# Kernel optimization log

Hardware: AMD Instinct MI355X
Metric: run time of the kernel (lower is better)

Reference implementation:

```python
import jax, jax.numpy as jnp
import numpy as np

B, N, STRIDE, NSAMPLE, RADIUS = 2, 8192, 4, 32, 0.1
CIN, COUT, LPC = 64, 128, 16
M = N // STRIDE
EPS = 1e-5


def conv1d(x, W, b=None):
    y = jnp.einsum('oc,bcn->bon', W, x)
    return y + b[None, :, None] if b is not None else y


def conv2d(x, W, b=None):
    y = jnp.einsum('oc,bcmk->bomk', W, x)
    return y + b[None, :, None, None] if b is not None else y


def bn(x, prm):
    # prm: [4, C] = (gamma, beta, running_mean, running_var); inference BN
    sh = (1, -1) + (1,) * (x.ndim - 2)
    g, be, m, v = (prm[i].reshape(sh) for i in range(4))
    return (x - m) * jax.lax.rsqrt(v + EPS) * g + be


def fps(p, m):
    # furthest point sampling, p: [B,N,3] -> idx [B,m] int32 (starts at index 0)
    b, n, _ = p.shape
    first = jnp.zeros((b,), jnp.int32)
    d0 = jnp.full((b, n), 1e10, p.dtype)

    def step(carry, _):
        dist, last = carry
        lastp = jnp.take_along_axis(p, jnp.broadcast_to(last[:, None, None], (b, 1, 3)), axis=1)
        dist = jnp.minimum(dist, jnp.sum((p - lastp) ** 2, -1))
        nxt = jnp.argmax(dist, -1).astype(jnp.int32)
        return (dist, nxt), nxt

    _, rest = jax.lax.scan(step, (d0, first), None, length=m - 1)
    return jnp.concatenate([first[:, None], rest.T], axis=1)


def ball_query(q, s, radius, ns):
    # q [B,M,3], s [B,N,3] -> neighbor indices [B,M,ns] (first ns points within radius, padded with first hit)
    n = s.shape[1]
    sqd = jnp.sum((q[:, :, None, :] - s[:, None, :, :]) ** 2, -1)  # [B,M,N]
    cand = jnp.where(sqd < radius * radius, jnp.arange(n, dtype=jnp.int32)[None, None, :], n)
    srt = jnp.sort(cand, axis=-1)[:, :, :ns]
    first = srt[:, :, :1]
    return jnp.where(srt == n, first, srt)


def group(feat, gidx):
    # feat [B,C,N], gidx [B,M,ns] -> [B,C,M,ns]
    return jax.vmap(lambda ft, gi: ft[:, gi])(feat, gidx)


def setup_inputs() -> dict:
    key = jax.random.key(0)
    ks = jax.random.split(key, 24)

    def w(k_, o, i):
        return jax.random.normal(k_, (o, i), jnp.float32) / np.sqrt(i).astype(np.float32)

    def bnp(k_, c):  # positive gamma/var, small-ish beta/mean
        return jax.random.uniform(k_, (4, c), jnp.float32) + 0.1

    return {
        'p': jax.random.uniform(ks[0], (B, N, 3), jnp.float32),
        'lp': jax.random.normal(ks[1], (B, LPC, N), jnp.float32),
        'f': jax.random.normal(ks[2], (B, CIN, N), jnp.float32),
        'W_skip': w(ks[3], COUT, CIN), 'b_skip': jax.random.normal(ks[4], (COUT,), jnp.float32) * 0.02,
        'W_post': w(ks[5], COUT, CIN), 'bn_post': bnp(ks[6], COUT),
        'W_loc1': w(ks[7], 32, LPC), 'bn_loc1': bnp(ks[8], 32),
        'W_loc2': w(ks[9], COUT, 32), 'bn_loc2': bnp(ks[10], COUT),
        'W_g': w(ks[11], 1, CIN), 'b_g': jax.random.normal(ks[12], (1,), jnp.float32) * 0.02,
        'W_v': w(ks[13], CIN, CIN), 'b_v': jax.random.normal(ks[14], (CIN,), jnp.float32) * 0.02,
        'W_w1': w(ks[15], CIN // 4, CIN), 'bn_w1': bnp(ks[16], CIN // 4),
        'W_w2': w(ks[17], CIN, CIN // 4), 'b_w2': jax.random.normal(ks[18], (CIN,), jnp.float32) * 0.02,
        'W_m': w(ks[19], COUT, CIN), 'bn_m': bnp(ks[20], COUT),
    }


def reference(p, lp, f, W_skip, b_skip, W_post, bn_post, W_loc1, bn_loc1, W_loc2, bn_loc2,
              W_g, b_g, W_v, b_v, W_w1, bn_w1, W_w2, b_w2, W_m, bn_m):
    b, n = p.shape[0], p.shape[1]
    m = n // STRIDE
    relu = jax.nn.relu

    # --- sampling + gathers ---
    idx = fps(p, m)  # [B,M]
    new_p = jnp.take_along_axis(p, jnp.broadcast_to(idx[:, :, None], (b, m, 3)), axis=1)
    fi = jnp.take_along_axis(f, jnp.broadcast_to(idx[:, None, :], (b, f.shape[1], m)), axis=2)
    lpi = jnp.take_along_axis(lp, jnp.broadcast_to(idx[:, None, :], (b, lp.shape[1], m)), axis=2)
    identity = conv1d(fi, W_skip, b_skip)  # [B,COUT,M]

    # --- global top-k relative-position attention branch ---
    att = jax.nn.sigmoid(conv1d(fi, W_g, b_g))  # [B,1,M]
    k = min(m // 4, 160)
    _, index_k = jax.lax.top_k(att[:, 0, :], k)  # [B,k]
    sparse_f = jnp.take_along_axis(fi, jnp.broadcast_to(index_k[:, None, :], (b, fi.shape[1], k)), axis=2)
    v = conv1d(sparse_f, W_v, b_v)  # [B,CIN,k]
    fi_att = fi * att
    r_qk = fi_att[:, :, :, None] - sparse_f[:, :, None, :]  # [B,CIN,M,k]
    r_qk = relu(bn(conv2d(r_qk, W_w1), bn_w1))
    r_qk = conv2d(r_qk, W_w2, b_w2)
    w_ = relu(r_qk)
    attfeat = jnp.mean(w_ * v[:, :, None, :], axis=-1)  # [B,CIN,M]
    global_f = relu(bn(conv1d(attfeat - fi, W_m), bn_m))  # [B,COUT,M]

    # --- local grouping branch ---
    fpost = relu(bn(conv1d(f, W_post), bn_post))  # [B,COUT,N]
    lpf = jnp.concatenate([lp, fpost], axis=1)  # [B,LPC+COUT,N]
    gidx = ball_query(new_p, p, RADIUS, NSAMPLE)  # [B,M,ns]
    lpfj = group(lpf, gidx)  # [B,LPC+COUT,M,ns]
    lpj, fj = lpfj[:, :LPC], lpfj[:, LPC:]
    dlpj = lpj - lpi[:, :, :, None]
    loc = relu(bn(conv2d(dlpj, W_loc1), bn_loc1))
    loc = relu(bn(conv2d(loc, W_loc2), bn_loc2))
    fout = jnp.max(fj + loc, axis=-1)  # [B,COUT,M]
    fout = fout + global_f
    fout = relu(fout + identity)
    return new_p, lpi, fout
```

## Files before the change

### kernel.cpp

```cpp
#include <hip/hip_runtime.h>
#include <stdint.h>

#define BB 2
#define NN 8192
#define MM 2048
#define CIN_ 64
#define COUT_ 128
#define LPC_ 16
#define NS_ 32
#define KSEL 160
#define EPSB 1e-5f

#define WS_IDX    0
#define WS_IDXK   4096
#define WS_LOGIT  4416
#define WS_ATT    8512
#define WS_FLAG   16380
#define WS_FIT    16384
#define WS_IDT    278528
#define WS_A1S    802816
#define WS_VT     868352
#define WS_B1S    888832
#define WS_GFT    893952
#define WS_FPOST  1418240
#define WS_GIDX   3515392

#define OUT_NEWP 0
#define OUT_LPI  12288
#define OUT_F    77824

typedef float    f16v __attribute__((ext_vector_type(16)));
typedef unsigned u16v __attribute__((ext_vector_type(16)));
typedef int      i16v __attribute__((ext_vector_type(16)));
typedef unsigned u8v  __attribute__((ext_vector_type(8)));

__device__ __forceinline__ float dist2_rn(float ax, float ay, float az,
                                          float bx, float by, float bz) {
  float dx = __fsub_rn(ax, bx);
  float dy = __fsub_rn(ay, by);
  float dz = __fsub_rn(az, bz);
  return __fadd_rn(__fadd_rn(__fmul_rn(dx, dx), __fmul_rn(dy, dy)), __fmul_rn(dz, dz));
}

template <int CTRL>
__device__ __forceinline__ unsigned long long dppmax64(unsigned long long x) {
  unsigned lo = (unsigned)x, hi = (unsigned)(x >> 32);
  unsigned plo = (unsigned)__builtin_amdgcn_update_dpp(0, (int)lo, CTRL, 0xF, 0xF, true);
  unsigned phi = (unsigned)__builtin_amdgcn_update_dpp(0, (int)hi, CTRL, 0xF, 0xF, true);
  unsigned long long o = ((unsigned long long)phi << 32) | plo;
  return o > x ? o : x;
}
#define DPP_XOR1 0xB1
#define DPP_XOR2 0x4E
#define DPP_HALFMIR 0x141
#define DPP_MIR 0x140
#define DPP_BC15 0x142
#define DPP_BC31 0x143

__device__ __forceinline__ unsigned mort4(unsigned x) {
  return (x & 1u) | ((x & 2u) << 2) | ((x & 4u) << 4) | ((x & 8u) << 6);
}

#define PPT 16
#define FPS_T 512
#define NWAVE 8
#define FPOST_BLKS ((BB * NN * 16) / FPS_T)
#define WARM_BLKS 254
#define WARM_CAP 4000

__global__ __launch_bounds__(FPS_T) void k_fps_fpost(const float* __restrict__ p,
                                                     int* __restrict__ idx_out,
                                                     float* __restrict__ newp_out,
                                                     const float* __restrict__ f,
                                                     const float* __restrict__ Wpost,
                                                     const float* __restrict__ bnpost,
                                                     float* __restrict__ fpostT,
                                                     int* __restrict__ flag) {
  __shared__ union {
    struct { unsigned int hist[4096]; unsigned int perm[NN]; } s;
    struct { float newp[MM * 3]; int idx[MM]; } o;
  } u;
  __shared__ unsigned long long slots[2][NWAVE];
  __shared__ float4 slotc[2][NWAVE];
  __shared__ unsigned int wsum[NWAVE];

  if (blockIdx.x >= 2 + FPOST_BLKS) {
    float a = 1.0000001f;
    float acc = (float)threadIdx.x;
    for (int it = 0; it < WARM_CAP; ++it) {
      if (__hip_atomic_load(flag, __ATOMIC_RELAXED, __HIP_MEMORY_SCOPE_AGENT) >= 2) break;
      #pragma unroll 64
      for (int k = 0; k < 512; ++k) acc = __builtin_fmaf(acc, a, 1.0f);
    }
    asm volatile("" ::"v"(acc));
    return;
  }

  if (blockIdx.x >= 2) {
    int gt = (blockIdx.x - 2) * FPS_T + threadIdx.x;
    int og = gt & 15, nn = gt >> 4;
    int b = nn >> 13, n = nn & 8191;
    const float* fb = f + b * CIN_ * NN + n;
    float acc[8];
    #pragma unroll
    for (int q = 0; q < 8; q++) acc[q] = 0.f;
    for (int c = 0; c < 64; c++) {
      float x = fb[c * NN];
      #pragma unroll
      for (int q = 0; q < 8; q++) acc[q] = fmaf(Wpost[(og * 8 + q) * 64 + c], x, acc[q]);
    }
    #pragma unroll
    for (int q = 0; q < 8; q++) {
      int o = og * 8 + q;
      float ga = bnpost[o], be = bnpost[COUT_ + o], mu = bnpost[2 * COUT_ + o],
            va = bnpost[3 * COUT_ + o];
      float sc = ga / sqrtf(va + EPSB);
      fpostT[(b * NN + n) * 128 + o] = fmaxf(acc[q] * sc + (be - mu * sc), 0.f);
    }
    return;
  }

  const int b = blockIdx.x;
  if (threadIdx.x == 0)
    __hip_atomic_store(flag, 0, __ATOMIC_RELAXED, __HIP_MEMORY_SCOPE_AGENT);
  const float* pb = p + b * NN * 3;
  const int tid = threadIdx.x;
  const int lane = tid & 63;
  const int wid = tid >> 6;

  for (int i = tid; i < 4096; i += FPS_T) u.s.hist[i] = 0u;
  __syncthreads();

  i16v cellv;
  #pragma unroll
  for (int k = 0; k < PPT; k++) {
    int i = tid + k * FPS_T;
    float x = pb[i * 3 + 0], y = pb[i * 3 + 1], z = pb[i * 3 + 2];
    int cx = (int)(x * 16.f); cx = cx < 0 ? 0 : (cx > 15 ? 15 : cx);
    int cy = (int)(y * 16.f); cy = cy < 0 ? 0 : (cy > 15 ? 15 : cy);
    int cz = (int)(z * 16.f); cz = cz < 0 ? 0 : (cz > 15 ? 15 : cz);
    int c = (int)(mort4((unsigned)cx) | (mort4((unsigned)cy) << 1) |
                  (mort4((unsigned)cz) << 2));
    cellv[k] = c;
    atomicAdd(&u.s.hist[c], 1u);
  }
  __syncthreads();

  u8v h;
  unsigned int s = 0;
  #pragma unroll
  for (int k = 0; k < 8; k++) { h[k] = u.s.hist[tid * 8 + k]; s += h[k]; }
  unsigned int pre = s;
  for (int d = 1; d < 64; d <<= 1) {
    unsigned int o = (unsigned int)__shfl_up((int)pre, d);
    if (lane >= d) pre += o;
  }
  if (lane == 63) wsum[wid] = pre;
  __syncthreads();
  if (tid < NWAVE) {
    unsigned int v = wsum[tid];
    unsigned int q = v;
    for (int d = 1; d < NWAVE; d <<= 1) {
      unsigned int o = (unsigned int)__shfl_up((int)q, d);
      if (tid >= d) q += o;
    }
    wsum[tid] = q - v;
  }
  __syncthreads();
  unsigned int base = wsum[wid] + (pre - s);
  #pragma unroll
  for (int k = 0; k < 8; k++) {
    u.s.hist[tid * 8 + k] = base;
    base += h[k];
  }
  __syncthreads();

  #pragma unroll
  for (int k = 0; k < PPT; k++) {
    unsigned int pos = atomicAdd(&u.s.hist[cellv[k]], 1u);
    u.s.perm[pos] = (unsigned int)(tid + k * FPS_T);
  }
  __syncthreads();

  f16v sx, sy, sz, dist;
  u16v lov;
  float bxmin = 1e30f, bymin = 1e30f, bzmin = 1e30f;
  float bxmax = -1e30f, bymax = -1e30f, bzmax = -1e30f;
  #pragma unroll
  for (int q = 0; q < PPT; q++) {
    unsigned int o = u.s.perm[tid * PPT + q];
    float x = pb[o * 3 + 0], y = pb[o * 3 + 1], z = pb[o * 3 + 2];
    sx[q] = x; sy[q] = y; sz[q] = z;
    lov[q] = ((8191u - o) << 4) | (unsigned int)q;
    dist[q] = 1e10f;
    bxmin = fminf(bxmin, x); bxmax = fmaxf(bxmax, x);
    bymin = fminf(bymin, y); bymax = fmaxf(bymax, y);
    bzmin = fminf(bzmin, z); bzmax = fmaxf(bzmax, z);
  }

  float wx = pb[0], wy = pb[1], wz = pb[2];
  unsigned long long thrPack = ((unsigned long long)__float_as_uint(1e10f) << 32);
  unsigned long long wpCache = 0ull;
  float scX = 0.f, scY = 0.f, scZ = 0.f;
  bool isPub = false;
  __syncthreads();

  if (tid == 0) {
    u.o.newp[0] = wx; u.o.newp[1] = wy; u.o.newp[2] = wz;
    u.o.idx[0] = 0;
  }

  for (int t = 1; t < MM; t++) {
    const int buf = t & 1;
    float ex = fmaxf(fmaxf(bxmin - wx, wx - bxmax), 0.f);
    float ey = fmaxf(fmaxf(bymin - wy, wy - bymax), 0.f);
    float ez = fmaxf(fmaxf(bzmin - wz, wz - bzmax), 0.f);
    float bd = (ex * ex + ey * ey + ez * ez) * 0.999f;
    float thrMax = __uint_as_float((unsigned int)(thrPack >> 32));
    bool active = (bd < thrMax);
    unsigned long long wmask = __ballot(active);
    if (wmask) {
      if (active) {
        unsigned long long best = 0ull;
        #pragma unroll
        for (int q = 0; q < PPT; q++) {
          float d = dist2_rn(sx[q], sy[q], sz[q], wx, wy, wz);
          float nd = fminf(dist[q], d);
          dist[q] = nd;
          unsigned long long pk =
              ((unsigned long long)__float_as_uint(nd) << 32) | (unsigned long long)lov[q];
          best = pk > best ? pk : best;
        }
        thrPack = best;
      }
      unsigned long long wp = thrPack;
      wp = dppmax64<DPP_XOR1>(wp);
      wp = dppmax64<DPP_XOR2>(wp);
      wp = dppmax64<DPP_HALFMIR>(wp);
      wp = dppmax64<DPP_MIR>(wp);
      wp = dppmax64<DPP_BC15>(wp);
      wp = dppmax64<DPP_BC31>(wp);
      unsigned wlo = (unsigned)__builtin_amdgcn_readlane((int)(unsigned)wp, 63);
      unsigned whi = (unsigned)__builtin_amdgcn_readlane((int)(unsigned)(wp >> 32), 63);
      unsigned long long wmax = ((unsigned long long)whi << 32) | wlo;
      isPub = (thrPack == wmax);
      if (isPub) {
        wpCache = wmax;
        unsigned qs = (unsigned)(wmax & 15ull);
        #pragma unroll
        for (int q = 0; q < PPT; q++) {
          if (qs == (unsigned)q) { scX = sx[q]; scY = sy[q]; scZ = sz[q]; }
        }
      }
    }
    if (isPub) {
      slots[buf][wid] = wpCache;
      slotc[buf][wid] = make_float4(scX, scY, scZ, 0.f);
    }
    __syncthreads();

    int sidx = lane & (NWAVE - 1);
    unsigned long long sp = slots[buf][sidx];
    float4 sc = slotc[buf][sidx];
    unsigned long long w2 = sp;
    w2 = dppmax64<DPP_XOR1>(w2);
    w2 = dppmax64<DPP_XOR2>(w2);
    w2 = dppmax64<DPP_HALFMIR>(w2);
    unsigned long long bal = __ballot(sp == w2);
    int src = __ffsll(bal) - 1;
    wx = __shfl(sc.x, src);
    wy = __shfl(sc.y, src);
    wz = __shfl(sc.z, src);
    if (tid == 0) {
      int worig = 8191 - (int)((w2 >> 4) & 0x1FFFull);
      u.o.newp[t * 3 + 0] = wx;
      u.o.newp[t * 3 + 1] = wy;
      u.o.newp[t * 3 + 2] = wz;
      u.o.idx[t] = worig;
    }
  }
  __syncthreads();

  for (int i = tid; i < MM * 3; i += FPS_T) newp_out[b * MM * 3 + i] = u.o.newp[i];
  for (int i = tid; i < MM; i += FPS_T) idx_out[b * MM + i] = u.o.idx[i];
  __syncthreads();
  if (tid == 0)
    __hip_atomic_fetch_add(flag, 1, __ATOMIC_RELEASE, __HIP_MEMORY_SCOPE_AGENT);
}

__global__ __launch_bounds__(256) void k_gather(const float* __restrict__ lp,
                                                const float* __restrict__ f,
                                                const int* __restrict__ idx,
                                                const float* __restrict__ Wg,
                                                const float* __restrict__ bg,
                                                float* __restrict__ fiT,
                                                float* __restrict__ logit,
                                                float* __restrict__ att,
                                                float* __restrict__ out_lpi) {
  int gm = blockIdx.x * 256 + threadIdx.x;
  if (gm >= BB * MM) return;
  int b = gm >> 11, m = gm & 2047;
  int j = idx[gm];
  const float* lpb = lp + b * LPC_ * NN;
  float* olpi = out_lpi + b * LPC_ * MM;
  #pragma unroll
  for (int c = 0; c < LPC_; c++) olpi[c * MM + m] = lpb[c * NN + j];
  const float* fb = f + b * CIN_ * NN;
  float lg = bg[0];
  #pragma unroll
  for (int c = 0; c < CIN_; c++) {
    float x = fb[c * NN + j];
    fiT[gm * 64 + c] = x;
    lg = __fadd_rn(lg, __fmul_rn(Wg[c], x));
  }
  logit[gm] = lg;
  att[gm] = 1.f / (1.f + expf(-lg));
}

__global__ __launch_bounds__(256) void k_ident(const float* __restrict__ fiT,
                                               const float* __restrict__ Wskip,
                                               const float* __restrict__ bskip,
                                               float* __restrict__ idT) {
  int gt = blockIdx.x * 256 + threadIdx.x;
  if (gt >= BB * MM * 16) return;
  int og = gt & 15, gm = gt >> 4;
  const float* fvp = fiT + gm * 64;
  #pragma unroll
  for (int q = 0; q < 8; q++) {
    int o = og * 8 + q;
    float a = bskip[o];
    #pragma unroll
    for (int c = 0; c < 64; c++) a = fmaf(Wskip[o * 64 + c], fvp[c], a);
    idT[gm * 128 + o] = a;
  }
}

__global__ __launch_bounds__(1024) void k_topk(const float* __restrict__ att,
                                               int* __restrict__ idxk) {
  __shared__ unsigned long long key[MM];
  int b = blockIdx.x, tid = threadIdx.x;
  for (int i = tid; i < MM; i += 1024) {
    unsigned int u = __float_as_uint(att[b * MM + i]);
    u ^= (u & 0x80000000u) ? 0xFFFFFFFFu : 0x80000000u;
    u = ~u;
    key[i] = ((unsigned long long)u << 32) | (unsigned int)i;
  }
  __syncthreads();
  for (int k = 2; k <= MM; k <<= 1) {
    for (int j = k >> 1; j > 0; j >>= 1) {
      for (int i = tid; i < MM; i += 1024) {
        int ixj = i ^ j;
        if (ixj > i) {
          bool up = (i & k) == 0;
          unsigned long long a = key[i], c = key[ixj];
          if ((a > c) == up) { key[i] = c; key[ixj] = a; }
        }
      }
      __syncthreads();
    }
  }
  if (tid < KSEL) idxk[b * KSEL + tid] = (int)(key[tid] & 0xFFFFFFFFull);
}

__global__ __launch_bounds__(256) void k_a1s(const float* __restrict__ fiT,
                                             const float* __restrict__ att,
                                             const float* __restrict__ Ww1,
                                             const float* __restrict__ bnw1,
                                             float* __restrict__ a1sT) {
  int gm = blockIdx.x * 256 + threadIdx.x;
  if (gm >= BB * MM) return;
  const float* fvp = fiT + gm * 64;
  float a = att[gm];
  #pragma unroll
  for (int c1 = 0; c1 < 16; c1++) {
    float acc = 0.f;
    #pragma unroll
    for (int c = 0; c < 64; c++) acc = fmaf(Ww1[c1 * 64 + c], fvp[c] * a, acc);
    float g = bnw1[c1], be = bnw1[16 + c1], mu = bnw1[32 + c1], va = bnw1[48 + c1];
    float sc = g / sqrtf(va + EPSB);
    a1sT[gm * 16 + c1] = acc * sc + (be - mu * sc);
  }
}

__global__ __launch_bounds__(256) void k_vb1(const float* __restrict__ fiT,
                                             const int* __restrict__ idxk,
                                             const float* __restrict__ Wv,
                                             const float* __restrict__ bv,
                                             const float* __restrict__ Ww1,
                                             const float* __restrict__ bnw1,
                                             float* __restrict__ vT,
                                             float* __restrict__ b1sT) {
  int gk = blockIdx.x * 256 + threadIdx.x;
  if (gk >= BB * KSEL) return;
  int b = gk / KSEL;
  int kk = idxk[gk];
  const float* fvp = fiT + (b * MM + kk) * 64;
  for (int o = 0; o < 64; o++) {
    float acc = bv[o];
    #pragma unroll
    for (int c = 0; c < 64; c++) acc = fmaf(Wv[o * 64 + c], fvp[c], acc);
    vT[gk * 64 + o] = acc;
  }
  #pragma unroll
  for (int c1 = 0; c1 < 16; c1++) {
    float acc = 0.f;
    #pragma unroll
    for (int c = 0; c < 64; c++) acc = fmaf(Ww1[c1 * 64 + c], fvp[c], acc);
    float g = bnw1[c1], va = bnw1[48 + c1];
    b1sT[gk * 16 + c1] = acc * (g / sqrtf(va + EPSB));
  }
}

__global__ __launch_bounds__(256) void k_att(const float* __restrict__ a1sT,
                                             const float* __restrict__ b1sT,
                                             const float* __restrict__ vT,
                                             const float* __restrict__ fiT,
                                             const float* __restrict__ Ww2,
                                             const float* __restrict__ bw2,
                                             const float* __restrict__ Wm,
                                             const float* __restrict__ bnm,
                                             float* __restrict__ gfT) {
  __shared__ float B1sh[KSEL * 16];
  __shared__ float dsh[4][64];
  int b = blockIdx.x >> 9;
  const float* bsrc = b1sT + b * KSEL * 16;
  for (int i = threadIdx.x; i < KSEL * 16; i += 256) B1sh[i] = bsrc[i];
  __syncthreads();
  int wid = threadIdx.x >> 6, lane = threadIdx.x & 63;
  int gm = blockIdx.x * 4 + wid;
  int c15 = lane & 15;
  float a1 = a1sT[gm * 16 + c15];
  f16v wrow;
  #pragma unroll
  for (int c = 0; c < 16; c++) wrow[c] = Ww2[lane * 16 + c];
  float bw = bw2[lane];
  const float* vp = vT + b * KSEL * 64 + lane;
  float acc = 0.f;
  for (int k = 0; k < KSEL; k++) {
    float t = fmaxf(a1 - B1sh[k * 16 + c15], 0.f);
    float r2 = bw;
    #pragma unroll
    for (int c = 0; c < 16; c++) {
      float tc = __int_as_float(__builtin_amdgcn_readlane(__float_as_int(t), c));
      r2 = fmaf(wrow[c], tc, r2);
    }
    acc = fmaf(fmaxf(r2, 0.f), vp[k * 64], acc);
  }
  float af = acc * (1.f / (float)KSEL);
  float d = af - fiT[gm * 64 + lane];
  dsh[wid][lane] = d;
  __syncthreads();
  #pragma unroll
  for (int t2 = 0; t2 < 2; t2++) {
    int o = lane + t2 * 64;
    float g = 0.f;
    #pragma unroll
    for (int c = 0; c < 64; c++) g = fmaf(Wm[o * 64 + c], dsh[wid][c], g);
    float ga = bnm[o], be = bnm[COUT_ + o], mu = bnm[2 * COUT_ + o], va = bnm[3 * COUT_ + o];
    float sc = ga / sqrtf(va + EPSB);
    gfT[gm * 128 + o] = fmaxf(g * sc + (be - mu * sc), 0.f);
  }
}

__global__ __launch_bounds__(256) void k_ball(const float* __restrict__ p,
                                              const float* __restrict__ newp,
                                              int* __restrict__ gidx) {
  int wid = threadIdx.x >> 6, lane = threadIdx.x & 63;
  int gm = blockIdx.x * 4 + wid;
  int b = gm >> 11;
  const float* q = newp + gm * 3;
  float qx = q[0], qy = q[1], qz = q[2];
  const float* pb = p + b * NN * 3;
  int* out = gidx + gm * NS_;
  const float RR = (float)(0.1 * 0.1);
  int cnt = 0, firstj = 0;
  bool haveFirst = false;
  for (int chunk = 0; chunk < NN / 64 && cnt < NS_; chunk++) {
    int j = chunk * 64 + lane;
    float d = dist2_rn(qx, qy, qz, pb[j * 3], pb[j * 3 + 1], pb[j * 3 + 2]);
    unsigned long long mask = __ballot(d < RR);
    while (mask && cnt < NS_) {
      int l = __ffsll(mask) - 1;
      mask &= mask - 1;
      int jj = chunk * 64 + l;
      if (!haveFirst) { firstj = jj; haveFirst = true; }
      if (lane == 0) out[cnt] = jj;
      cnt++;
    }
  }
  if (lane == 0) {
    for (int i = cnt; i < NS_; i++) out[i] = firstj;
  }
}

__global__ __launch_bounds__(128) void k_final(const float* __restrict__ lp,
                                               const float* __restrict__ lpi_out,
                                               const int* __restrict__ gidx,
                                               const float* __restrict__ Wl1,
                                               const float* __restrict__ bnl1,
                                               const float* __restrict__ Wl2,
                                               const float* __restrict__ bnl2,
                                               const float* __restrict__ fpostT,
                                               const float* __restrict__ gfT,
                                               const float* __restrict__ idT,
                                               float* __restrict__ out_f) {
  __shared__ float loc1[NS_][32];
  __shared__ float dls[NS_][16];
  int gm = blockIdx.x;
  int b = gm >> 11, m = gm & 2047;
  int tid = threadIdx.x;
  const int* gx = gidx + gm * NS_;
  for (int i = tid; i < NS_ * 16; i += 128) {
    int s = i >> 4, c = i & 15;
    int j = gx[s];
    dls[s][c] = lp[(b * LPC_ + c) * NN + j] - lpi_out[(b * LPC_ + c) * MM + m];
  }
  __syncthreads();
  for (int i = tid; i < NS_ * 32; i += 128) {
    int s = i >> 5, o = i & 31;
    float a = 0.f;
    #pragma unroll
    for (int c = 0; c < 16; c++) a = fmaf(Wl1[o * 16 + c], dls[s][c], a);
    float ga = bnl1[o], be = bnl1[32 + o], mu = bnl1[64 + o], va = bnl1[96 + o];
    float sc = ga / sqrtf(va + EPSB);
    loc1[s][o] = fmaxf(a * sc + (be - mu * sc), 0.f);
  }
  __syncthreads();
  f16v wr0, wr1;
  #pragma unroll
  for (int c = 0; c < 16; c++) { wr0[c] = Wl2[tid * 32 + c]; wr1[c] = Wl2[tid * 32 + 16 + c]; }
  float ga = bnl2[tid], be = bnl2[128 + tid], mu = bnl2[256 + tid], va = bnl2[384 + tid];
  float sc = ga / sqrtf(va + EPSB);
  float sh = be - mu * sc;
  float mx = -1e30f;
  for (int s = 0; s < NS_; s++) {
    float g = 0.f;
    #pragma unroll
    for (int c = 0; c < 16; c++) g = fmaf(wr0[c], loc1[s][c], g);
    #pragma unroll
    for (int c = 0; c < 16; c++) g = fmaf(wr1[c], loc1[s][16 + c], g);
    float l2 = fmaxf(g * sc + sh, 0.f);
    int j = gx[s];
    float fj = fpostT[(b * NN + j) * 128 + tid];
    mx = fmaxf(mx, fj + l2);
  }
  float fout = fmaxf(mx + gfT[gm * 128 + tid] + idT[gm * 128 + tid], 0.f);
  out_f[(b * COUT_ + tid) * MM + m] = fout;
}

extern "C" void kernel_launch(void* const* d_in, const int* in_sizes, int n_in,
                              void* d_out, int out_size, void* d_ws, size_t ws_size,
                              hipStream_t stream) {
  (void)in_sizes; (void)n_in; (void)out_size; (void)ws_size;
  const float* p      = (const float*)d_in[0];
  const float* lp     = (const float*)d_in[1];
  const float* f      = (const float*)d_in[2];
  const float* W_skip = (const float*)d_in[3];
  const float* b_skip = (const float*)d_in[4];
  const float* W_post = (const float*)d_in[5];
  const float* bn_post= (const float*)d_in[6];
  const float* W_loc1 = (const float*)d_in[7];
  const float* bn_loc1= (const float*)d_in[8];
  const float* W_loc2 = (const float*)d_in[9];
  const float* bn_loc2= (const float*)d_in[10];
  const float* W_g    = (const float*)d_in[11];
  const float* b_g    = (const float*)d_in[12];
  const float* W_v    = (const float*)d_in[13];
  const float* b_v    = (const float*)d_in[14];
  const float* W_w1   = (const float*)d_in[15];
  const float* bn_w1  = (const float*)d_in[16];
  const float* W_w2   = (const float*)d_in[17];
  const float* b_w2   = (const float*)d_in[18];
  const float* W_m    = (const float*)d_in[19];
  const float* bn_m   = (const float*)d_in[20];

  float* out = (float*)d_out;
  float* ws = (float*)d_ws;
  int*   idx    = (int*)(ws + WS_IDX);
  int*   idxk   = (int*)(ws + WS_IDXK);
  float* att    = ws + WS_ATT;
  int*   flag   = (int*)(ws + WS_FLAG);
  float* fiT    = ws + WS_FIT;
  float* idT    = ws + WS_IDT;
  float* a1sT   = ws + WS_A1S;
  float* vT     = ws + WS_VT;
  float* b1sT   = ws + WS_B1S;
  float* gfT    = ws + WS_GFT;
  float* fpostT = ws + WS_FPOST;
  float* logit  = ws + WS_LOGIT;
  int*   gidx   = (int*)(ws + WS_GIDX);

  k_fps_fpost<<<2 + FPOST_BLKS + WARM_BLKS, FPS_T, 0, stream>>>(p, idx, out + OUT_NEWP, f,
                                                                W_post, bn_post, fpostT, flag);
  k_gather<<<(BB * MM + 255) / 256, 256, 0, stream>>>(lp, f, idx, W_g, b_g, fiT, logit, att,
                                                      out + OUT_LPI);
  k_ident<<<(BB * MM * 16) / 256, 256, 0, stream>>>(fiT, W_skip, b_skip, idT);
  k_topk<<<BB, 1024, 0, stream>>>(att, idxk);
  k_a1s<<<(BB * MM + 255) / 256, 256, 0, stream>>>(fiT, att, W_w1, bn_w1, a1sT);
  k_vb1<<<(BB * KSEL + 255) / 256, 256, 0, stream>>>(fiT, idxk, W_v, b_v, W_w1, bn_w1, vT, b1sT);
  k_att<<<(BB * MM) / 4, 256, 0, stream>>>(a1sT, b1sT, vT, fiT, W_w2, b_w2, W_m, bn_m, gfT);
  k_ball<<<(BB * MM) / 4, 256, 0, stream>>>(p, out + OUT_NEWP, gidx);
  k_final<<<BB * MM, 128, 0, stream>>>(lp, out + OUT_LPI, gidx, W_loc1, bn_loc1, W_loc2, bn_loc2,
                                       fpostT, gfT, idT, out + OUT_F);
}
```

Measured before the change: 2.295 ms.

## Keep FPS point coordinates in LDS and look up winner by packed slot

Moves the sorted point coordinates out of per-thread registers into shared memory (xy as float2, z separately). The packed key now carries the owning thread and slot, so after the block-wide max every lane reads the winner's coordinates straight from LDS. This removes the coordinate-publish slots, the ballot/shuffle broadcast and the per-wave select loop. It also splits the per-thread max into four independent chains and moves the new_p output write into the gather kernel. The aim is to shorten each serial FPS iteration and lower register pressure, at the cost of extra LDS reads in the inner loop.

Result: no change. 2.324 ms (+1.3%).

```diff
diff --git a/kernel.cpp b/kernel.cpp
--- a/kernel.cpp
+++ b/kernel.cpp
@@ -70,18 +70,21 @@
 
 __global__ __launch_bounds__(FPS_T) void k_fps_fpost(const float* __restrict__ p,
                                                      int* __restrict__ idx_out,
-                                                     float* __restrict__ newp_out,
                                                      const float* __restrict__ f,
                                                      const float* __restrict__ Wpost,
                                                      const float* __restrict__ bnpost,
                                                      float* __restrict__ fpostT,
                                                      int* __restrict__ flag) {
-  __shared__ union {
-    struct { unsigned int hist[4096]; unsigned int perm[NN]; } s;
-    struct { float newp[MM * 3]; int idx[MM]; } o;
-  } u;
+  __shared__ float2 xyl[NN];
+  __shared__ union UZ {
+    float zz[NN];
+    struct { float zlow[NN - 4096]; unsigned short perm[NN]; } s;
+  } uz;
+  __shared__ union UH {
+    unsigned int hist[4096];
+    int idxs[MM];
+  } uh;
   __shared__ unsigned long long slots[2][NWAVE];
-  __shared__ float4 slotc[2][NWAVE];
   __shared__ unsigned int wsum[NWAVE];
 
   if (blockIdx.x >= 2 + FPOST_BLKS) {
@@ -128,7 +131,7 @@
   const int lane = tid & 63;
   const int wid = tid >> 6;
 
-  for (int i = tid; i < 4096; i += FPS_T) u.s.hist[i] = 0u;
+  for (int i = tid; i < 4096; i += FPS_T) uh.hist[i] = 0u;
   __syncthreads();
 
   i16v cellv;
@@ -142,14 +145,14 @@
     int c = (int)(mort4((unsigned)cx) | (mort4((unsigned)cy) << 1) |
                   (mort4((unsigned)cz) << 2));
     cellv[k] = c;
-    atomicAdd(&u.s.hist[c], 1u);
+    atomicAdd(&uh.hist[c], 1u);
   }
   __syncthreads();
 
   u8v h;
   unsigned int s = 0;
   #pragma unroll
-  for (int k = 0; k < 8; k++) { h[k] = u.s.hist[tid * 8 + k]; s += h[k]; }
+  for (int k = 0; k < 8; k++) { h[k] = uh.hist[tid * 8 + k]; s += h[k]; }
   unsigned int pre = s;
   for (int d = 1; d < 64; d <<= 1) {
     unsigned int o = (unsigned int)__shfl_up((int)pre, d);
@@ -170,28 +173,34 @@
   unsigned int base = wsum[wid] + (pre - s);
   #pragma unroll
   for (int k = 0; k < 8; k++) {
-    u.s.hist[tid * 8 + k] = base;
+    uh.hist[tid * 8 + k] = base;
     base += h[k];
   }
   __syncthreads();
 
   #pragma unroll
   for (int k = 0; k < PPT; k++) {
-    unsigned int pos = atomicAdd(&u.s.hist[cellv[k]], 1u);
-    u.s.perm[pos] = (unsigned int)(tid + k * FPS_T);
-  }
-  __syncthreads();
-
-  f16v sx, sy, sz, dist;
+    unsigned int pos = atomicAdd(&uh.hist[cellv[k]], 1u);
+    uz.s.perm[pos] = (unsigned short)(tid + k * FPS_T);
+  }
+  __syncthreads();
+
+  u16v porig;
+  #pragma unroll
+  for (int q = 0; q < PPT; q++) porig[q] = uz.s.perm[tid * PPT + q];
+  __syncthreads();
+
+  f16v dist;
   u16v lov;
   float bxmin = 1e30f, bymin = 1e30f, bzmin = 1e30f;
   float bxmax = -1e30f, bymax = -1e30f, bzmax = -1e30f;
   #pragma unroll
   for (int q = 0; q < PPT; q++) {
-    unsigned int o = u.s.perm[tid * PPT + q];
+    unsigned int o = porig[q];
     float x = pb[o * 3 + 0], y = pb[o * 3 + 1], z = pb[o * 3 + 2];
-    sx[q] = x; sy[q] = y; sz[q] = z;
-    lov[q] = ((8191u - o) << 4) | (unsigned int)q;
+    xyl[q * FPS_T + tid] = make_float2(x, y);
+    uz.zz[q * FPS_T + tid] = z;
+    lov[q] = ((8191u - o) << 13) | ((unsigned)tid << 4) | (unsigned)q;
     dist[q] = 1e10f;
     bxmin = fminf(bxmin, x); bxmax = fmaxf(bxmax, x);
     bymin = fminf(bymin, y); bymax = fmaxf(bymax, y);
@@ -200,15 +209,9 @@
 
   float wx = pb[0], wy = pb[1], wz = pb[2];
   unsigned long long thrPack = ((unsigned long long)__float_as_uint(1e10f) << 32);
-  unsigned long long wpCache = 0ull;
-  float scX = 0.f, scY = 0.f, scZ = 0.f;
-  bool isPub = false;
-  __syncthreads();
-
-  if (tid == 0) {
-    u.o.newp[0] = wx; u.o.newp[1] = wy; u.o.newp[2] = wz;
-    u.o.idx[0] = 0;
-  }
+  __syncthreads();
+
+  if (tid == 0) uh.idxs[0] = 0;
 
   for (int t = 1; t < MM; t++) {
     const int buf = t & 1;
@@ -218,77 +221,62 @@
     float bd = (ex * ex + ey * ey + ez * ez) * 0.999f;
     float thrMax = __uint_as_float((unsigned int)(thrPack >> 32));
     bool active = (bd < thrMax);
-    unsigned long long wmask = __ballot(active);
-    if (wmask) {
-      if (active) {
-        unsigned long long best = 0ull;
-        #pragma unroll
-        for (int q = 0; q < PPT; q++) {
-          float d = dist2_rn(sx[q], sy[q], sz[q], wx, wy, wz);
-          float nd = fminf(dist[q], d);
-          dist[q] = nd;
-          unsigned long long pk =
-              ((unsigned long long)__float_as_uint(nd) << 32) | (unsigned long long)lov[q];
-          best = pk > best ? pk : best;
-        }
-        thrPack = best;
+    if (active) {
+      unsigned long long m0 = 0ull, m1 = 0ull, m2 = 0ull, m3 = 0ull;
+      #pragma unroll
+      for (int q = 0; q < PPT; q++) {
+        float2 a = xyl[q * FPS_T + tid];
+        float az = uz.zz[q * FPS_T + tid];
+        float d = dist2_rn(a.x, a.y, az, wx, wy, wz);
+        float nd = fminf(dist[q], d);
+        dist[q] = nd;
+        unsigned long long pk =
+            ((unsigned long long)__float_as_uint(nd) << 32) | (unsigned long long)lov[q];
+        if ((q & 3) == 0) m0 = pk > m0 ? pk : m0;
+        else if ((q & 3) == 1) m1 = pk > m1 ? pk : m1;
+        else if ((q & 3) == 2) m2 = pk > m2 ? pk : m2;
+        else m3 = pk > m3 ? pk : m3;
       }
-      unsigned long long wp = thrPack;
-      wp = dppmax64<DPP_XOR1>(wp);
-      wp = dppmax64<DPP_XOR2>(wp);
-      wp = dppmax64<DPP_HALFMIR>(wp);
-      wp = dppmax64<DPP_MIR>(wp);
-      wp = dppmax64<DPP_BC15>(wp);
-      wp = dppmax64<DPP_BC31>(wp);
-      unsigned wlo = (unsigned)__builtin_amdgcn_readlane((int)(unsigned)wp, 63);
-      unsigned whi = (unsigned)__builtin_amdgcn_readlane((int)(unsigned)(wp >> 32), 63);
-      unsigned long long wmax = ((unsigned long long)whi << 32) | wlo;
-      isPub = (thrPack == wmax);
-      if (isPub) {
-        wpCache = wmax;
-        unsigned qs = (unsigned)(wmax & 15ull);
-        #pragma unroll
-        for (int q = 0; q < PPT; q++) {
-          if (qs == (unsigned)q) { scX = sx[q]; scY = sy[q]; scZ = sz[q]; }
-        }
-      }
-    }
-    if (isPub) {
-      slots[buf][wid] = wpCache;
-      slotc[buf][wid] = make_float4(scX, scY, scZ, 0.f);
-    }
+      unsigned long long ba = m0 > m1 ? m0 : m1;
+      unsigned long long bb2 = m2 > m3 ? m2 : m3;
+      thrPack = ba > bb2 ? ba : bb2;
+    }
+    unsigned long long wp = thrPack;
+    wp = dppmax64<DPP_XOR1>(wp);
+    wp = dppmax64<DPP_XOR2>(wp);
+    wp = dppmax64<DPP_HALFMIR>(wp);
+    wp = dppmax64<DPP_MIR>(wp);
+    wp = dppmax64<DPP_BC15>(wp);
+    wp = dppmax64<DPP_BC31>(wp);
+    unsigned wlo = (unsigned)__builtin_amdgcn_readlane((int)(unsigned)wp, 63);
+    unsigned whi = (unsigned)__builtin_amdgcn_readlane((int)(unsigned)(wp >> 32), 63);
+    unsigned long long wmax = ((unsigned long long)whi << 32) | wlo;
+    if (thrPack == wmax) slots[buf][wid] = wmax;
     __syncthreads();
 
     int sidx = lane & (NWAVE - 1);
-    unsigned long long sp = slots[buf][sidx];
-    float4 sc = slotc[buf][sidx];
-    unsigned long long w2 = sp;
+    unsigned long long w2 = slots[buf][sidx];
     w2 = dppmax64<DPP_XOR1>(w2);
     w2 = dppmax64<DPP_XOR2>(w2);
     w2 = dppmax64<DPP_HALFMIR>(w2);
-    unsigned long long bal = __ballot(sp == w2);
-    int src = __ffsll(bal) - 1;
-    wx = __shfl(sc.x, src);
-    wy = __shfl(sc.y, src);
-    wz = __shfl(sc.z, src);
-    if (tid == 0) {
-      int worig = 8191 - (int)((w2 >> 4) & 0x1FFFull);
-      u.o.newp[t * 3 + 0] = wx;
-      u.o.newp[t * 3 + 1] = wy;
-      u.o.newp[t * 3 + 2] = wz;
-      u.o.idx[t] = worig;
-    }
-  }
-  __syncthreads();
-
-  for (int i = tid; i < MM * 3; i += FPS_T) newp_out[b * MM * 3 + i] = u.o.newp[i];
-  for (int i = tid; i < MM; i += FPS_T) idx_out[b * MM + i] = u.o.idx[i];
+    unsigned lo32 = (unsigned)w2;
+    int tidwin = (int)((lo32 >> 4) & 511u);
+    int qwin = (int)(lo32 & 15u);
+    float2 cw = xyl[qwin * FPS_T + tidwin];
+    float zw = uz.zz[qwin * FPS_T + tidwin];
+    wx = cw.x; wy = cw.y; wz = zw;
+    if (tid == 0) uh.idxs[t] = 8191 - (int)((lo32 >> 13) & 0x1FFFu);
+  }
+  __syncthreads();
+
+  for (int i = tid; i < MM; i += FPS_T) idx_out[b * MM + i] = uh.idxs[i];
   __syncthreads();
   if (tid == 0)
     __hip_atomic_fetch_add(flag, 1, __ATOMIC_RELEASE, __HIP_MEMORY_SCOPE_AGENT);
 }
 
-__global__ __launch_bounds__(256) void k_gather(const float* __restrict__ lp,
+__global__ __launch_bounds__(256) void k_gather(const float* __restrict__ p,
+                                                const float* __restrict__ lp,
                                                 const float* __restrict__ f,
                                                 const int* __restrict__ idx,
                                                 const float* __restrict__ Wg,
@@ -296,11 +284,15 @@
                                                 float* __restrict__ fiT,
                                                 float* __restrict__ logit,
                                                 float* __restrict__ att,
-                                                float* __restrict__ out_lpi) {
+                                                float* __restrict__ out_lpi,
+                                                float* __restrict__ out_newp) {
   int gm = blockIdx.x * 256 + threadIdx.x;
   if (gm >= BB * MM) return;
   int b = gm >> 11, m = gm & 2047;
   int j = idx[gm];
+  out_newp[gm * 3 + 0] = p[(b * NN + j) * 3 + 0];
+  out_newp[gm * 3 + 1] = p[(b * NN + j) * 3 + 1];
+  out_newp[gm * 3 + 2] = p[(b * NN + j) * 3 + 2];
   const float* lpb = lp + b * LPC_ * NN;
   float* olpi = out_lpi + b * LPC_ * MM;
   #pragma unroll
@@ -590,10 +582,10 @@
   float* logit  = ws + WS_LOGIT;
   int*   gidx   = (int*)(ws + WS_GIDX);
 
-  k_fps_fpost<<<2 + FPOST_BLKS + WARM_BLKS, FPS_T, 0, stream>>>(p, idx, out + OUT_NEWP, f,
-                                                                W_post, bn_post, fpostT, flag);
-  k_gather<<<(BB * MM + 255) / 256, 256, 0, stream>>>(lp, f, idx, W_g, b_g, fiT, logit, att,
-                                                      out + OUT_LPI);
+  k_fps_fpost<<<2 + FPOST_BLKS + WARM_BLKS, FPS_T, 0, stream>>>(p, idx, f, W_post, bn_post,
+                                                                fpostT, flag);
+  k_gather<<<(BB * MM + 255) / 256, 256, 0, stream>>>(p, lp, f, idx, W_g, b_g, fiT, logit, att,
+                                                      out + OUT_LPI, out + OUT_NEWP);
   k_ident<<<(BB * MM * 16) / 256, 256, 0, stream>>>(fiT, W_skip, b_skip, idT);
   k_topk<<<BB, 1024, 0, stream>>>(att, idxk);
   k_a1s<<<(BB * MM + 255) / 256, 256, 0, stream>>>(fiT, att, W_w1, bn_w1, a1sT);
```
